# Kernel optimization log

Hardware: AMD Instinct MI355X
Metric: run time of the kernel (lower is better)

## Reference

```python
import jax, jax.numpy as jnp
import numpy as np

NUM_HEADS = 8

def setup_inputs() -> dict:
    key = jax.random.key(0)
    k1, k2, k3, k4, k5 = jax.random.split(key, 5)
    B, N, C = 4, 2048, 512
    x = jax.random.normal(k1, (B, N, C), dtype=jnp.float32)
    s = 1.0 / np.sqrt(C)
    qkv_w = jax.random.uniform(k2, (3 * C, C), dtype=jnp.float32, minval=-s, maxval=s)
    qkv_b = jax.random.uniform(k3, (3 * C,), dtype=jnp.float32, minval=-s, maxval=s)
    proj_w = jax.random.uniform(k4, (C, C), dtype=jnp.float32, minval=-s, maxval=s)
    proj_b = jax.random.uniform(k5, (C,), dtype=jnp.float32, minval=-s, maxval=s)
    return {"x": x, "qkv_w": qkv_w, "qkv_b": qkv_b, "proj_w": proj_w, "proj_b": proj_b}

def reference(x, qkv_w, qkv_b, proj_w, proj_b):
    B, N, C = x.shape
    H = NUM_HEADS
    D = C // H
    scale = D ** -0.5
    # qkv: [B,N,3C] -> [3,B,H,N,D]
    qkv = (jnp.einsum('bnc,oc->bno', x, qkv_w) + qkv_b)
    qkv = qkv.reshape(B, N, 3, H, D).transpose(2, 0, 3, 1, 4)
    q, k, v = qkv[0], qkv[1], qkv[2]
    attn = jnp.einsum('bhnd,bhmd->bhnm', q, k) * scale  # [B,H,N,N]
    attn = jax.nn.softmax(attn, axis=-1)
    out = jnp.einsum('bhnm,bhmd->bhnd', attn, v)  # [B,H,N,D]
    out = out.transpose(0, 2, 1, 3).reshape(B, N, C)
    return jnp.einsum('bnc,oc->bno', out, proj_w) + proj_b
```

## Files before the change

kernel.cpp:

```cpp
#include <hip/hip_runtime.h>
#include <stdint.h>


typedef short bf16x8 __attribute__((ext_vector_type(8)));
typedef float f32x2  __attribute__((ext_vector_type(2)));
typedef float f32x4  __attribute__((ext_vector_type(4)));
typedef float f32x16 __attribute__((ext_vector_type(16)));
typedef unsigned int u32x4 __attribute__((ext_vector_type(4)));

__device__ __forceinline__ unsigned short f2bf(float f) {
    unsigned int u = __builtin_bit_cast(unsigned int, f);
    u += 0x7fffu + ((u >> 16) & 1u);
    return (unsigned short)(u >> 16);
}
__device__ __forceinline__ unsigned int pk2(float a, float b) {
    return (unsigned int)f2bf(a) | ((unsigned int)f2bf(b) << 16);
}
__device__ __forceinline__ float fexp2(float x) {
    return __builtin_amdgcn_exp2f(x);
}
__device__ __forceinline__ bf16x8 ld8_f32(const float* __restrict__ p) {
    float4 f0 = *(const float4*)p;
    float4 f1 = *(const float4*)(p + 4);
    u32x4 u = {pk2(f0.x, f0.y), pk2(f0.z, f0.w), pk2(f1.x, f1.y), pk2(f1.z, f1.w)};
    return __builtin_bit_cast(bf16x8, u);
}
__device__ __forceinline__ void async16(const void* g, void* l) {
    __builtin_amdgcn_global_load_lds(
        (const __attribute__((address_space(1))) unsigned int*)g,
        (__attribute__((address_space(3))) unsigned int*)l,
        16, 0, 0);
}

#define MFMA16(a, b, c) __builtin_amdgcn_mfma_f32_16x16x32_bf16((a), (b), (c), 0, 0, 0)
#define MFMA32(a, b, c) __builtin_amdgcn_mfma_f32_32x32x16_bf16((a), (b), (c), 0, 0, 0)

__global__ void cvt_bf16(const float* __restrict__ x,
                         const float* __restrict__ w,
                         const float* __restrict__ w2,
                         unsigned short* __restrict__ xb,
                         unsigned short* __restrict__ wb,
                         unsigned short* __restrict__ wb2)
{
    const int G = 524288 + 98304 + 32768;
    for (int idx = blockIdx.x * 256 + threadIdx.x; idx < G; idx += gridDim.x * 256) {
        if (idx < 524288)
            *(bf16x8*)(xb + (size_t)idx * 8) = ld8_f32(x + (size_t)idx * 8);
        else if (idx < 524288 + 98304) {
            int j = idx - 524288;
            *(bf16x8*)(wb + (size_t)j * 8) = ld8_f32(w + (size_t)j * 8);
        } else {
            int j = idx - 524288 - 98304;
            *(bf16x8*)(wb2 + (size_t)j * 8) = ld8_f32(w2 + (size_t)j * 8);
        }
    }
}

__global__ __launch_bounds__(256, 4)
void gemm_qkv(const unsigned short* __restrict__ A,
              const unsigned short* __restrict__ B,
              const float* __restrict__ bias,
              unsigned short* __restrict__ out0,
              unsigned short* __restrict__ out1,
              unsigned short* __restrict__ out2,
              int K)
{
    __shared__ unsigned short sA[128 * 32];
    __shared__ unsigned short sB[128 * 32];

    const int tid  = threadIdx.x;
    const int wave = tid >> 6, lane = tid & 63;
    const int l = lane & 15, q16 = lane >> 4;
    const int wm = wave >> 1, wn = wave & 1;
    const int bid = blockIdx.x;
    const int slot = bid >> 3;
    const int m0 = ((bid & 7) * 8 + slot / 12) * 128;
    const int n0 = (slot % 12) * 128;

    f32x4 acc[4][4];
#pragma unroll
    for (int i = 0; i < 4; ++i)
#pragma unroll
        for (int j = 0; j < 4; ++j)
            acc[i][j] = (f32x4){0.f, 0.f, 0.f, 0.f};

    for (int k0 = 0; k0 < K; k0 += 32) {
#pragma unroll
        for (int call = 0; call < 2; ++call) {
            int L = call * 256 + tid;
            int r = L >> 2, c = L & 3;
            async16(A + (size_t)(m0 + r) * K + k0 + c * 8, sA + L * 8);
            async16(B + (size_t)(n0 + r) * K + k0 + c * 8, sB + L * 8);
        }
        __syncthreads();

        bf16x8 af[4], bfr[4];
#pragma unroll
        for (int i = 0; i < 4; ++i)
            af[i] = *(const bf16x8*)(sA + ((wm * 64 + i * 16 + l) * 4 + q16) * 8);
#pragma unroll
        for (int j = 0; j < 4; ++j)
            bfr[j] = *(const bf16x8*)(sB + ((wn * 64 + j * 16 + l) * 4 + q16) * 8);
#pragma unroll
        for (int i = 0; i < 4; ++i)
#pragma unroll
            for (int j = 0; j < 4; ++j)
                acc[i][j] = MFMA16(af[i], bfr[j], acc[i][j]);
        __syncthreads();
    }

    const float lscale = 0.18033688f;
#pragma unroll
    for (int i = 0; i < 4; ++i) {
#pragma unroll
        for (int j = 0; j < 4; ++j) {
            int col = n0 + wn * 64 + j * 16 + l;
            float bv = bias[col];
#pragma unroll
            for (int r = 0; r < 4; ++r) {
                int row = m0 + wm * 64 + i * 16 + q16 * 4 + r;
                float val = acc[i][j][r] + bv;
                int which = col >> 9;
                int h = (col >> 6) & 7, d = col & 63;
                int b = row >> 11, n = row & 2047;
                if (which == 0)
                    out0[(size_t)(((b * 8 + h) * 2048) + n) * 64 + d] = f2bf(val * lscale);
                else if (which == 1)
                    out1[(size_t)(((b * 8 + h) * 2048) + n) * 64 + d] = f2bf(val);
                else {
                    int np = (n & ~12) | ((n & 8) >> 1) | ((n & 4) << 1);
                    out2[(size_t)(((b * 8 + h) * 64) + d) * 2048 + np] = f2bf(val);
                }
            }
        }
    }
}

__global__ __launch_bounds__(256, 4)
void gemm_out(const unsigned short* __restrict__ A,
              const unsigned short* __restrict__ B,
              const float* __restrict__ bias,
              float* __restrict__ outf,
              int K, int N)
{
    __shared__ unsigned short sA[64 * 32];
    __shared__ unsigned short sB[128 * 32];

    const int tid  = threadIdx.x;
    const int wave = tid >> 6, lane = tid & 63;
    const int l = lane & 15, q16 = lane >> 4;
    const int wm = wave >> 1, wn = wave & 1;
    const int bid = blockIdx.x;
    const int slot = bid >> 3;
    const int m0 = ((bid & 7) * 16 + (slot >> 2)) * 64;
    const int n0 = (slot & 3) * 128;

    f32x4 acc[2][4];
#pragma unroll
    for (int i = 0; i < 2; ++i)
#pragma unroll
        for (int j = 0; j < 4; ++j)
            acc[i][j] = (f32x4){0.f, 0.f, 0.f, 0.f};

    for (int k0 = 0; k0 < K; k0 += 32) {
        {
            int r = tid >> 2, c = tid & 3;
            async16(A + (size_t)(m0 + r) * K + k0 + c * 8, sA + tid * 8);
        }
#pragma unroll
        for (int call = 0; call < 2; ++call) {
            int L = call * 256 + tid;
            int r = L >> 2, c = L & 3;
            async16(B + (size_t)(n0 + r) * K + k0 + c * 8, sB + L * 8);
        }
        __syncthreads();

        bf16x8 af[2], bfr[4];
#pragma unroll
        for (int i = 0; i < 2; ++i)
            af[i] = *(const bf16x8*)(sA + ((wm * 32 + i * 16 + l) * 4 + q16) * 8);
#pragma unroll
        for (int j = 0; j < 4; ++j)
            bfr[j] = *(const bf16x8*)(sB + ((wn * 64 + j * 16 + l) * 4 + q16) * 8);
#pragma unroll
        for (int i = 0; i < 2; ++i)
#pragma unroll
            for (int j = 0; j < 4; ++j)
                acc[i][j] = MFMA16(af[i], bfr[j], acc[i][j]);
        __syncthreads();
    }

#pragma unroll
    for (int i = 0; i < 2; ++i) {
#pragma unroll
        for (int j = 0; j < 4; ++j) {
            int col = n0 + wn * 64 + j * 16 + l;
            float bv = bias[col];
#pragma unroll
            for (int r = 0; r < 4; ++r) {
                int row = m0 + wm * 32 + i * 16 + q16 * 4 + r;
                outf[(size_t)row * N + col] = acc[i][j][r] + bv;
            }
        }
    }
}

__global__ __launch_bounds__(256, 2)
void attn_fused(const unsigned short* __restrict__ Q,
                const unsigned short* __restrict__ Km,
                const unsigned short* __restrict__ Vt,
                unsigned short* __restrict__ O)
{
    __shared__ unsigned short sK[2][128 * 64];
    __shared__ unsigned short sVt[2][64 * 128];

    const int tid  = threadIdx.x;
    const int wave = tid >> 6, lane = tid & 63;
    const int l31 = lane & 31, h = lane >> 5;
    const int swz = l31 & 7;
    const int qh = wave & 1, kh = wave >> 1;
    const int bid = blockIdx.x;
    const int slot = bid >> 3;
    const int bh = (bid & 7) * 4 + (slot >> 4);
    const int n0 = (slot & 15) * 128;
    const int q0 = n0 + qh * 64;

    const unsigned short* Kp = Km + (size_t)bh * 2048 * 64;
    const unsigned short* Vp = Vt + (size_t)bh * 64 * 2048;
    const unsigned short* sKf = &sK[0][0];
    const unsigned short* sVf = &sVt[0][0];

    int ka[4], va[2][2];
#pragma unroll
    for (int ks = 0; ks < 4; ++ks)
        ka[ks] = (kh * 64 + l31) * 64 + ((ks * 2 + h) ^ swz) * 8;
#pragma unroll
    for (int m1 = 0; m1 < 2; ++m1)
#pragma unroll
        for (int ks2 = 0; ks2 < 2; ++ks2)
            va[m1][ks2] = l31 * 128 + ((m1 * 4 + ks2 * 2 + h) ^ swz) * 8 + kh * 64;

    int ksrc[4], vsrc[4], dst[4];
#pragma unroll
    for (int c = 0; c < 4; ++c) {
        int s = wave * 256 + c * 64 + lane;
        int rk = s >> 3;
        ksrc[c] = rk * 64 + ((s & 7) ^ (rk & 7)) * 8;
        int rv = s >> 4;
        vsrc[c] = rv * 2048 + ((s & 15) ^ (rv & 7)) * 8;
        dst[c] = s * 8;
    }

    bf16x8 qf[2][4];
#pragma unroll
    for (int qt = 0; qt < 2; ++qt)
#pragma unroll
        for (int ks = 0; ks < 4; ++ks)
            qf[qt][ks] = *(const bf16x8*)(Q + (size_t)(bh * 2048 + q0 + qt * 32 + l31) * 64
                                          + ks * 16 + h * 8);

    f32x16 oacc[2][2];
#pragma unroll
    for (int qt = 0; qt < 2; ++qt)
#pragma unroll
        for (int dt = 0; dt < 2; ++dt)
#pragma unroll
            for (int e = 0; e < 16; ++e) oacc[qt][dt][e] = 0.f;
    f32x16 Zv;
#pragma unroll
    for (int e = 0; e < 16; ++e) Zv[e] = 0.f;
    f32x2 l2[2];
    l2[0] = (f32x2){0.f, 0.f};
    l2[1] = (f32x2){0.f, 0.f};

#pragma unroll
    for (int c = 0; c < 4; ++c) {
        async16(Kp + ksrc[c], (void*)(sKf + dst[c]));
        async16(Vp + vsrc[c], (void*)(sVf + dst[c]));
    }
    __syncthreads();

    for (int it = 0; it < 16; ++it) {
        const int nb = ((it + 1) & 1) * 8192;
        if (it < 15) {
            int kv = (it + 1) * 128;
#pragma unroll
            for (int c = 0; c < 4; ++c)
                async16(Kp + (size_t)kv * 64 + ksrc[c], (void*)(sKf + nb + dst[c]));
        }

        f32x16 sacc[2][2];
#pragma unroll
        for (int mt = 0; mt < 2; ++mt) {
            bf16x8 kf0 = *(const bf16x8*)(sKf + ka[0] + mt * 2048);
            sacc[0][mt] = MFMA32(kf0, qf[0][0], Zv);
            sacc[1][mt] = MFMA32(kf0, qf[1][0], Zv);
#pragma unroll
            for (int ks = 1; ks < 4; ++ks) {
                bf16x8 kf = *(const bf16x8*)(sKf + ka[ks] + mt * 2048);
                sacc[0][mt] = MFMA32(kf, qf[0][ks], sacc[0][mt]);
                sacc[1][mt] = MFMA32(kf, qf[1][ks], sacc[1][mt]);
            }
        }

        if (it < 15) {
            int kv = (it + 1) * 128;
#pragma unroll
            for (int c = 0; c < 4; ++c)
                async16(Vp + (size_t)kv + vsrc[c], (void*)(sVf + nb + dst[c]));
        }

#pragma unroll
        for (int mt = 0; mt < 2; ++mt) {
            unsigned int pk[2][4][2];
#pragma unroll
            for (int qt = 0; qt < 2; ++qt) {
#pragma unroll
                for (int g = 0; g < 4; ++g) {
                    float p0 = fexp2(sacc[qt][mt][4 * g + 0]);
                    float p1 = fexp2(sacc[qt][mt][4 * g + 1]);
                    float p2 = fexp2(sacc[qt][mt][4 * g + 2]);
                    float p3 = fexp2(sacc[qt][mt][4 * g + 3]);
                    l2[qt] += (f32x2){p0, p1};
                    l2[qt] += (f32x2){p2, p3};
                    pk[qt][g][0] = __builtin_amdgcn_perm(
                        __builtin_bit_cast(unsigned int, p1),
                        __builtin_bit_cast(unsigned int, p0), 0x07060302u);
                    pk[qt][g][1] = __builtin_amdgcn_perm(
                        __builtin_bit_cast(unsigned int, p3),
                        __builtin_bit_cast(unsigned int, p2), 0x07060302u);
                }
            }
#pragma unroll
            for (int ks2 = 0; ks2 < 2; ++ks2) {
                u32x4 bu0, bu1;
                bu0[0] = pk[0][2 * ks2][0];
                bu0[1] = pk[0][2 * ks2][1];
                bu0[2] = pk[0][2 * ks2 + 1][0];
                bu0[3] = pk[0][2 * ks2 + 1][1];
                bu1[0] = pk[1][2 * ks2][0];
                bu1[1] = pk[1][2 * ks2][1];
                bu1[2] = pk[1][2 * ks2 + 1][0];
                bu1[3] = pk[1][2 * ks2 + 1][1];
                bf16x8 bf0 = __builtin_bit_cast(bf16x8, bu0);
                bf16x8 bf1 = __builtin_bit_cast(bf16x8, bu1);
#pragma unroll
                for (int dt = 0; dt < 2; ++dt) {
                    bf16x8 vf = *(const bf16x8*)(sVf + va[mt][ks2] + dt * 4096);
                    oacc[0][dt] = MFMA32(vf, bf0, oacc[0][dt]);
                    oacc[1][dt] = MFMA32(vf, bf1, oacc[1][dt]);
                }
            }
        }

#pragma unroll
        for (int ks = 0; ks < 4; ++ks) ka[ks] ^= 8192;
        va[0][0] ^= 8192; va[0][1] ^= 8192; va[1][0] ^= 8192; va[1][1] ^= 8192;
        __syncthreads();
    }

    float* sf = (float*)&sK[0][0];
    float* sl = (float*)&sVt[0][0];
    if (kh == 1) {
        const int base = (qh * 64 + lane) * 64;
#pragma unroll
        for (int qt = 0; qt < 2; ++qt)
#pragma unroll
            for (int dt = 0; dt < 2; ++dt) {
                int chunk = (qt * 2 + dt) ^ (lane & 3);
                *(f32x16*)(sf + base + chunk * 16) = oacc[qt][dt];
            }
        *(f32x2*)(sl + (qh * 64 + lane) * 4 + 0) = l2[0];
        *(f32x2*)(sl + (qh * 64 + lane) * 4 + 2) = l2[1];
    }
    __syncthreads();
    if (kh == 0) {
        const int base = (qh * 64 + lane) * 64;
#pragma unroll
        for (int qt = 0; qt < 2; ++qt)
#pragma unroll
            for (int dt = 0; dt < 2; ++dt) {
                int chunk = (qt * 2 + dt) ^ (lane & 3);
                f32x16 part = *(const f32x16*)(sf + base + chunk * 16);
#pragma unroll
                for (int e = 0; e < 16; ++e) oacc[qt][dt][e] += part[e];
            }
        l2[0] += *(const f32x2*)(sl + (qh * 64 + lane) * 4 + 0);
        l2[1] += *(const f32x2*)(sl + (qh * 64 + lane) * 4 + 2);

        const int b = bh >> 3, hh = bh & 7;
#pragma unroll
        for (int qt = 0; qt < 2; ++qt) {
            float l_run = l2[qt][0] + l2[qt][1];
            l_run += __shfl_xor(l_run, 32);
            float inv = 1.f / fmaxf(l_run, 1e-20f);
            unsigned short* obase = O + ((size_t)(b * 2048 + q0 + qt * 32 + l31)) * 512 + hh * 64;
#pragma unroll
            for (int dt = 0; dt < 2; ++dt)
#pragma unroll
                for (int g = 0; g < 4; ++g) {
                    int d = dt * 32 + 8 * g + 4 * h;
                    unsigned int w0 = pk2(oacc[qt][dt][4 * g + 0] * inv,
                                          oacc[qt][dt][4 * g + 1] * inv);
                    unsigned int w1 = pk2(oacc[qt][dt][4 * g + 2] * inv,
                                          oacc[qt][dt][4 * g + 3] * inv);
                    uint2 w = {w0, w1};
                    *(uint2*)(obase + d) = w;
                }
        }
    }
}

extern "C" void kernel_launch(void* const* d_in, const int* in_sizes, int n_in,
                              void* d_out, int out_size, void* d_ws, size_t ws_size,
                              hipStream_t stream)
{
    const float* x      = (const float*)d_in[0];
    const float* qkv_w  = (const float*)d_in[1];
    const float* qkv_b  = (const float*)d_in[2];
    const float* proj_w = (const float*)d_in[3];
    const float* proj_b = (const float*)d_in[4];

    const size_t PER = 4u * 8u * 2048u * 64u;
    unsigned short* q_ws  = (unsigned short*)d_ws;
    unsigned short* k_ws  = q_ws  + PER;
    unsigned short* vt_ws = k_ws  + PER;
    unsigned short* ao_ws = vt_ws + PER;
    unsigned short* wb2   = ao_ws + PER;

    unsigned short* xb = (unsigned short*)d_out;
    unsigned short* wb = xb + PER;

    cvt_bf16<<<dim3(640), 256, 0, stream>>>(x, qkv_w, proj_w, xb, wb, wb2);
    gemm_qkv<<<dim3(768), 256, 0, stream>>>(xb, wb, qkv_b, q_ws, k_ws, vt_ws, 512);
    attn_fused<<<dim3(512), 256, 0, stream>>>(q_ws, k_ws, vt_ws, ao_ws);
    gemm_out<<<dim3(512), 256, 0, stream>>>(ao_ws, wb2, proj_b, (float*)d_out, 512, 512);
}
```

Baseline: 156.0 us.

## Widen attention blocks to 8 waves with triple-buffered K/V prefetch

The attention kernel now runs 512-thread blocks that each cover 256 queries, with 4 query groups and 2 KV halves, so every K/V tile loaded into LDS is reused by twice as many query rows. LDS becomes a triple-buffered ring, and K and V are prefetched two tiles ahead. Manual vmcnt waits plus raw s_barrier replace the __syncthreads at the end of each iteration. MFMA issue is wrapped in s_setprio to favour matrix work. This cuts global K/V traffic and barrier stalls, but raises LDS use to 96KB per block, which may limit occupancy, and the grid is halved to 256 blocks.

```diff
diff --git a/kernel.cpp b/kernel.cpp
--- a/kernel.cpp
+++ b/kernel.cpp
@@ -205,30 +205,29 @@
     }
 }
 
-__global__ __launch_bounds__(256, 2)
+__global__ __launch_bounds__(512, 2)
 void attn_fused(const unsigned short* __restrict__ Q,
                 const unsigned short* __restrict__ Km,
                 const unsigned short* __restrict__ Vt,
                 unsigned short* __restrict__ O)
 {
-    __shared__ unsigned short sK[2][128 * 64];
-    __shared__ unsigned short sVt[2][64 * 128];
+    __shared__ unsigned short sAll[49152];
 
     const int tid  = threadIdx.x;
     const int wave = tid >> 6, lane = tid & 63;
     const int l31 = lane & 31, h = lane >> 5;
     const int swz = l31 & 7;
-    const int qh = wave & 1, kh = wave >> 1;
+    const int qq = wave >> 1, kh = wave & 1;
     const int bid = blockIdx.x;
     const int slot = bid >> 3;
-    const int bh = (bid & 7) * 4 + (slot >> 4);
-    const int n0 = (slot & 15) * 128;
-    const int q0 = n0 + qh * 64;
+    const int bh = (bid & 7) * 4 + (slot >> 3);
+    const int qc = slot & 7;
+    const int q0 = qc * 256 + qq * 64;
 
     const unsigned short* Kp = Km + (size_t)bh * 2048 * 64;
     const unsigned short* Vp = Vt + (size_t)bh * 64 * 2048;
-    const unsigned short* sKf = &sK[0][0];
-    const unsigned short* sVf = &sVt[0][0];
+    unsigned short* sKf = sAll;
+    unsigned short* sVf = sAll + 24576;
 
     int ka[4], va[2][2];
 #pragma unroll
@@ -240,15 +239,15 @@
         for (int ks2 = 0; ks2 < 2; ++ks2)
             va[m1][ks2] = l31 * 128 + ((m1 * 4 + ks2 * 2 + h) ^ swz) * 8 + kh * 64;
 
-    int ksrc[4], vsrc[4], dst[4];
-#pragma unroll
-    for (int c = 0; c < 4; ++c) {
-        int s = wave * 256 + c * 64 + lane;
+    int ksrc[2], vsrc[2], dsl[2];
+#pragma unroll
+    for (int c = 0; c < 2; ++c) {
+        int s = c * 512 + tid;
         int rk = s >> 3;
         ksrc[c] = rk * 64 + ((s & 7) ^ (rk & 7)) * 8;
         int rv = s >> 4;
         vsrc[c] = rv * 2048 + ((s & 15) ^ (rv & 7)) * 8;
-        dst[c] = s * 8;
+        dsl[c] = s * 8;
     }
 
     bf16x8 qf[2][4];
@@ -274,40 +273,49 @@
     l2[1] = (f32x2){0.f, 0.f};
 
 #pragma unroll
-    for (int c = 0; c < 4; ++c) {
-        async16(Kp + ksrc[c], (void*)(sKf + dst[c]));
-        async16(Vp + vsrc[c], (void*)(sVf + dst[c]));
-    }
-    __syncthreads();
+    for (int c = 0; c < 2; ++c) {
+        async16(Kp + ksrc[c], (void*)(sKf + dsl[c]));
+        async16(Vp + vsrc[c], (void*)(sVf + dsl[c]));
+    }
+#pragma unroll
+    for (int c = 0; c < 2; ++c) {
+        async16(Kp + (size_t)128 * 64 + ksrc[c], (void*)(sKf + 8192 + dsl[c]));
+        async16(Vp + (size_t)128 + vsrc[c], (void*)(sVf + 8192 + dsl[c]));
+    }
+    asm volatile("s_waitcnt vmcnt(4)" ::: "memory");
+    __builtin_amdgcn_s_barrier();
+    __builtin_amdgcn_sched_barrier(0);
+
+    int off0 = 0, off1 = 8192, off2 = 16384;
 
     for (int it = 0; it < 16; ++it) {
-        const int nb = ((it + 1) & 1) * 8192;
-        if (it < 15) {
-            int kv = (it + 1) * 128;
-#pragma unroll
-            for (int c = 0; c < 4; ++c)
-                async16(Kp + (size_t)kv * 64 + ksrc[c], (void*)(sKf + nb + dst[c]));
-        }
-
+        if (it < 14) {
+            size_t kv = (size_t)(it + 2) * 128;
+#pragma unroll
+            for (int c = 0; c < 2; ++c) {
+                async16(Kp + kv * 64 + ksrc[c], (void*)(sKf + off2 + dsl[c]));
+                async16(Vp + kv + vsrc[c], (void*)(sVf + off2 + dsl[c]));
+            }
+        }
+
+        const unsigned short* sKc = sKf + off0;
+        const unsigned short* sVc = sVf + off0;
         f32x16 sacc[2][2];
 #pragma unroll
         for (int mt = 0; mt < 2; ++mt) {
-            bf16x8 kf0 = *(const bf16x8*)(sKf + ka[0] + mt * 2048);
+            bf16x8 kf0 = *(const bf16x8*)(sKc + ka[0] + mt * 2048);
+            __builtin_amdgcn_s_setprio(1);
             sacc[0][mt] = MFMA32(kf0, qf[0][0], Zv);
             sacc[1][mt] = MFMA32(kf0, qf[1][0], Zv);
+            __builtin_amdgcn_s_setprio(0);
 #pragma unroll
             for (int ks = 1; ks < 4; ++ks) {
-                bf16x8 kf = *(const bf16x8*)(sKf + ka[ks] + mt * 2048);
+                bf16x8 kf = *(const bf16x8*)(sKc + ka[ks] + mt * 2048);
+                __builtin_amdgcn_s_setprio(1);
                 sacc[0][mt] = MFMA32(kf, qf[0][ks], sacc[0][mt]);
                 sacc[1][mt] = MFMA32(kf, qf[1][ks], sacc[1][mt]);
-            }
-        }
-
-        if (it < 15) {
-            int kv = (it + 1) * 128;
-#pragma unroll
-            for (int c = 0; c < 4; ++c)
-                async16(Vp + (size_t)kv + vsrc[c], (void*)(sVf + nb + dst[c]));
+                __builtin_amdgcn_s_setprio(0);
+            }
         }
 
 #pragma unroll
@@ -346,23 +354,34 @@
                 bf16x8 bf1 = __builtin_bit_cast(bf16x8, bu1);
 #pragma unroll
                 for (int dt = 0; dt < 2; ++dt) {
-                    bf16x8 vf = *(const bf16x8*)(sVf + va[mt][ks2] + dt * 4096);
+                    bf16x8 vf = *(const bf16x8*)(sVc + va[mt][ks2] + dt * 4096);
+                    __builtin_amdgcn_s_setprio(1);
                     oacc[0][dt] = MFMA32(vf, bf0, oacc[0][dt]);
                     oacc[1][dt] = MFMA32(vf, bf1, oacc[1][dt]);
+                    __builtin_amdgcn_s_setprio(0);
                 }
             }
         }
 
-#pragma unroll
-        for (int ks = 0; ks < 4; ++ks) ka[ks] ^= 8192;
-        va[0][0] ^= 8192; va[0][1] ^= 8192; va[1][0] ^= 8192; va[1][1] ^= 8192;
-        __syncthreads();
-    }
-
-    float* sf = (float*)&sK[0][0];
-    float* sl = (float*)&sVt[0][0];
+        if (it < 14) {
+            asm volatile("s_waitcnt vmcnt(4)" ::: "memory");
+        } else if (it == 14) {
+            asm volatile("s_waitcnt vmcnt(0)" ::: "memory");
+        }
+        if (it < 15) {
+            asm volatile("s_waitcnt lgkmcnt(0)" ::: "memory");
+            __builtin_amdgcn_s_barrier();
+            __builtin_amdgcn_sched_barrier(0);
+        }
+
+        int t = off0; off0 = off1; off1 = off2; off2 = t;
+    }
+
+    __syncthreads();
+    float* sf = (float*)sAll;
+    float* sl = sf + 16384;
     if (kh == 1) {
-        const int base = (qh * 64 + lane) * 64;
+        const int base = (qq * 64 + lane) * 64;
 #pragma unroll
         for (int qt = 0; qt < 2; ++qt)
 #pragma unroll
@@ -370,12 +389,12 @@
                 int chunk = (qt * 2 + dt) ^ (lane & 3);
                 *(f32x16*)(sf + base + chunk * 16) = oacc[qt][dt];
             }
-        *(f32x2*)(sl + (qh * 64 + lane) * 4 + 0) = l2[0];
-        *(f32x2*)(sl + (qh * 64 + lane) * 4 + 2) = l2[1];
+        *(f32x2*)(sl + (qq * 64 + lane) * 4 + 0) = l2[0];
+        *(f32x2*)(sl + (qq * 64 + lane) * 4 + 2) = l2[1];
     }
     __syncthreads();
     if (kh == 0) {
-        const int base = (qh * 64 + lane) * 64;
+        const int base = (qq * 64 + lane) * 64;
 #pragma unroll
         for (int qt = 0; qt < 2; ++qt)
 #pragma unroll
@@ -385,8 +404,8 @@
 #pragma unroll
                 for (int e = 0; e < 16; ++e) oacc[qt][dt][e] += part[e];
             }
-        l2[0] += *(const f32x2*)(sl + (qh * 64 + lane) * 4 + 0);
-        l2[1] += *(const f32x2*)(sl + (qh * 64 + lane) * 4 + 2);
+        l2[0] += *(const f32x2*)(sl + (qq * 64 + lane) * 4 + 0);
+        l2[1] += *(const f32x2*)(sl + (qq * 64 + lane) * 4 + 2);
 
         const int b = bh >> 3, hh = bh & 7;
 #pragma unroll
@@ -433,6 +452,6 @@
 
     cvt_bf16<<<dim3(640), 256, 0, stream>>>(x, qkv_w, proj_w, xb, wb, wb2);
     gemm_qkv<<<dim3(768), 256, 0, stream>>>(xb, wb, qkv_b, q_ws, k_ws, vt_ws, 512);
-    attn_fused<<<dim3(512), 256, 0, stream>>>(q_ws, k_ws, vt_ws, ao_ws);
+    attn_fused<<<dim3(256), 512, 0, stream>>>(q_ws, k_ws, vt_ws, ao_ws);
     gemm_out<<<dim3(512), 256, 0, stream>>>(ao_ws, wb2, proj_b, (float*)d_out, 512, 512);
 }
```

After: 154.1 us. No clear change (-1.2%).
